# Kernel tuning notes

Measured on AMD Instinct MI355X. Metric: run time of the kernel, lower is better.

Reference implementation:

```python
import jax, jax.numpy as jnp
import numpy as np

N = 50000      # nodes
C = 64         # in_channels
O = 64         # out_channels (== in_channels, required by zeros_like in original)
S = 8          # size: number of weight matrices
E = 1700000    # edges (neighbor pairs incl. self-loops), avg degree ~34


def setup_inputs() -> dict:
    key = jax.random.key(0)
    ks = jax.random.split(key, 9)
    node_tensor = jax.random.normal(ks[0], (N, C), dtype=jnp.float32)
    src = jax.random.randint(ks[1], (E,), 0, N)                 # neighbor node j
    dst = jnp.sort(jax.random.randint(ks[2], (E,), 0, N))       # center node i
    sc = 1.0 / np.sqrt(C)
    W = jax.random.normal(ks[3], (S, C, O), dtype=jnp.float32) * sc   # linears weights
    b = jax.random.normal(ks[4], (S, O), dtype=jnp.float32) * sc      # linears biases
    Ws = jax.random.normal(ks[5], (C, S), dtype=jnp.float32) * sc     # source proj
    bs = jax.random.normal(ks[6], (S,), dtype=jnp.float32) * sc
    Wt = jax.random.normal(ks[7], (C, S), dtype=jnp.float32) * sc     # target proj
    bt = jax.random.normal(ks[8], (S,), dtype=jnp.float32) * sc
    return dict(node_tensor=node_tensor, src=src, dst=dst,
                W=W, b=b, Ws=Ws, bs=bs, Wt=Wt, bt=bt)


def reference(node_tensor, src, dst, W, b, Ws, bs, Wt, bt):
    # Per-node soft-assignment logits (FeaStNet)
    s = node_tensor @ Ws + bs          # [N, S] : source_tensor
    t = node_tensor @ Wt + bt          # [N, S] : target_tensor
    # Per-edge assignment: softmax over the `size` dim of source[center] + target[neighbor]
    q = jax.nn.softmax(s[dst] + t[src], axis=-1)      # [E, S]
    # Per-matrix projected node features: weighted[m] = x @ W_m + b_m
    Wx = jnp.einsum('nc,sco->sno', node_tensor, W) + b[:, None, :]   # [S, N, O]
    # msg[e] = sum_m q[e,m] * Wx[m, src[e]]; loop over small fixed S to avoid [S,E,O] blowup
    msg = q[:, 0:1] * Wx[0][src]                      # [E, O]
    for m in range(1, S):
        msg = msg + q[:, m:m + 1] * Wx[m][src]
    # Scatter-sum over each center's neighborhood, mean over the S weight matrices
    out = jax.ops.segment_sum(msg, dst, num_segments=N) / S          # [N, O]
    return out
```

## Files before the change

kernel.cpp:

```cpp
#include <hip/hip_runtime.h>
#include <hip/hip_bf16.h>


#define CDIM 64
#define SDIM 8

typedef __bf16 bf16x8 __attribute__((ext_vector_type(8)));
typedef __bf16 bf16x4 __attribute__((ext_vector_type(4)));
typedef float f32x4 __attribute__((ext_vector_type(4)));

__global__ __launch_bounds__(256) void k1_pre(
    const float* __restrict__ x, const float* __restrict__ Ws,
    const float* __restrict__ bs, const float* __restrict__ Wt,
    const float* __restrict__ bt, const float* __restrict__ W,
    const int* __restrict__ dst, float* __restrict__ ST,
    __hip_bfloat16* __restrict__ xbf, __hip_bfloat16* __restrict__ WtB,
    int* __restrict__ rowptr, int N, int E, int nbN) {
  int bid = blockIdx.x;
  if (bid >= nbN + 128) {
    int e = (bid - nbN - 128) * 256 + threadIdx.x;
    if (e >= E) return;
    int a = dst[e];
    int bnd = (e + 1 < E) ? dst[e + 1] : N;
    if (e == 0) {
      for (int d = 0; d <= a; ++d) rowptr[d] = 0;
    }
    for (int d = a + 1; d <= bnd; ++d) rowptr[d] = e + 1;
    return;
  }
  if (bid >= nbN) {
    int t = (bid - nbN) * 256 + threadIdx.x;
    int o = t >> 9, k = t & 511;
    WtB[t] = __float2bfloat16(W[(size_t)k * 64 + o]);
    return;
  }

  __shared__ __hip_bfloat16 wst[16 * 72];
  __shared__ float bst[16];
  int t = threadIdx.x;
#pragma unroll
  for (int j = 0; j < 4; ++j) {
    int idx = t * 4 + j;
    int n = idx >> 6, k = idx & 63;
    float v = (n < 8) ? Ws[k * 8 + n] : Wt[k * 8 + (n - 8)];
    wst[n * 72 + k] = __float2bfloat16(v);
  }
  if (t < 16) bst[t] = (t < 8) ? bs[t] : bt[t - 8];
  __syncthreads();

  int wave = t >> 6, lane = t & 63;
  int r = lane & 15, q = lane >> 4;
  int node = bid * 64 + wave * 16 + r;
  int nodec = node < N ? node : N - 1;
  const float* xr = x + (size_t)nodec * CDIM;

  bf16x8 afrag[2];
#pragma unroll
  for (int kt = 0; kt < 2; ++kt) {
    float4 u0 = *(const float4*)(xr + kt * 32 + q * 8);
    float4 u1 = *(const float4*)(xr + kt * 32 + q * 8 + 4);
    union { bf16x8 v; __hip_bfloat16 h[8]; } a;
    a.h[0] = __float2bfloat16(u0.x); a.h[1] = __float2bfloat16(u0.y);
    a.h[2] = __float2bfloat16(u0.z); a.h[3] = __float2bfloat16(u0.w);
    a.h[4] = __float2bfloat16(u1.x); a.h[5] = __float2bfloat16(u1.y);
    a.h[6] = __float2bfloat16(u1.z); a.h[7] = __float2bfloat16(u1.w);
    afrag[kt] = a.v;
    if (node < N)
      *(bf16x8*)(xbf + (size_t)node * CDIM + kt * 32 + q * 8) = a.v;
  }

  bf16x8 bf0 = *(const bf16x8*)(wst + r * 72 + q * 8);
  bf16x8 bf1 = *(const bf16x8*)(wst + r * 72 + 32 + q * 8);

  f32x4 acc = {0, 0, 0, 0};
  acc = __builtin_amdgcn_mfma_f32_16x16x32_bf16(afrag[0], bf0, acc, 0, 0, 0);
  acc = __builtin_amdgcn_mfma_f32_16x16x32_bf16(afrag[1], bf1, acc, 0, 0, 0);

  int m = lane & 15;
#pragma unroll
  for (int v = 0; v < 4; ++v) {
    int nd = bid * 64 + wave * 16 + q * 4 + v;
    if (nd >= N) continue;
    float val = acc[v] + bst[m];
    if (m >= 8) val = __expf(val);
    ST[nd * 16 + m] = val;
  }
}

__global__ __launch_bounds__(256, 4) void k3_mfma(
    const __hip_bfloat16* __restrict__ xbf, const int* __restrict__ src,
    const int* __restrict__ rowptr, const float* __restrict__ ST,
    __hip_bfloat16* __restrict__ Gbf, float* __restrict__ R, int N) {
  __shared__ __hip_bfloat16 qt_s[4][16 * 40];
  __shared__ __hip_bfloat16 xt_s[4][4 * 32 * 16];

  int wave = threadIdx.x >> 6;
  int lane = threadIdx.x & 63;
  int i = blockIdx.x * 4 + wave;
  if (i >= N) return;

  int mm = lane & 7;
  int kk = lane >> 3;
  int mp = lane & 15;
  int q3 = lane >> 4;

  __hip_bfloat16* qt = &qt_s[wave][0];
  __hip_bfloat16* xt = &xt_s[wave][0];

  __hip_bfloat16 z0 = __float2bfloat16(0.0f);
#pragma unroll
  for (int z = 0; z < 5; ++z) qt[320 + z * 64 + lane] = z0;

  int lo = rowptr[i];
  int hi = rowptr[i + 1];
  float uv = __expf(ST[i * 16 + mm]);

  unsigned rd_addr = (unsigned)(uintptr_t)xt + (unsigned)q3 * 256u +
                     (unsigned)mp * 8u;
  __hip_bfloat16* xw = xt + (mm >> 1) * 512 + (mm & 1) * 8;

  f32x4 acc0 = {0, 0, 0, 0}, acc1 = {0, 0, 0, 0};
  f32x4 acc2 = {0, 0, 0, 0}, acc3 = {0, 0, 0, 0};
  float racc = 0.f;

  if (lo < hi) {
    int ecl = hi - 1;
    int iv[4], niv[4];
    bf16x8 xv[4];
    float tv[4];

#pragma unroll
    for (int g = 0; g < 4; ++g) {
      int ek = lo + g * 8 + kk;
      iv[g] = src[ek < ecl ? ek : ecl];
    }
#pragma unroll
    for (int g = 0; g < 4; ++g)
      xv[g] = *(const bf16x8*)(xbf + (size_t)iv[g] * CDIM + mm * 8);
#pragma unroll
    for (int g = 0; g < 4; ++g) tv[g] = ST[iv[g] * 16 + 8 + mm];
    if (lo + 32 < hi) {
#pragma unroll
      for (int g = 0; g < 4; ++g) {
        int ek = lo + 32 + g * 8 + kk;
        niv[g] = src[ek < ecl ? ek : ecl];
      }
    }

    for (int c0 = lo; c0 < hi; c0 += 32) {
      bool hasn = (c0 + 32 < hi);
      bf16x8 nxv[4];
      float ntv[4];
      int nniv[4];
      if (hasn) {
#pragma unroll
        for (int g = 0; g < 4; ++g)
          nxv[g] = *(const bf16x8*)(xbf + (size_t)niv[g] * CDIM + mm * 8);
#pragma unroll
        for (int g = 0; g < 4; ++g) ntv[g] = ST[niv[g] * 16 + 8 + mm];
        if (c0 + 64 < hi) {
#pragma unroll
          for (int g = 0; g < 4; ++g) {
            int ek = c0 + 64 + g * 8 + kk;
            nniv[g] = src[ek < ecl ? ek : ecl];
          }
        }
      }

#pragma unroll
      for (int g = 0; g < 4; ++g) {
        float w = uv * tv[g];
        float ssum = w + __shfl_xor(w, 1);
        ssum += __shfl_xor(ssum, 2);
        ssum += __shfl_xor(ssum, 4);
        float qv = w * __frcp_rn(ssum);
        if (c0 + g * 8 + kk >= hi) qv = 0.f;
        racc += qv;
        qt[mm * 40 + g * 8 + kk] = __float2bfloat16(qv);
      }

#pragma unroll
      for (int g = 0; g < 4; ++g)
        *(bf16x8*)(xw + (g * 8 + kk) * 16) = xv[g];

      bf16x8 afrag = *(const bf16x8*)(qt + mp * 40 + q3 * 8);

      bf16x4 t0, t1, t2, t3, t4, t5, t6, t7;
      asm volatile(
          "ds_read_b64_tr_b16 %0, %8 offset:0\n\t"
          "ds_read_b64_tr_b16 %1, %8 offset:128\n\t"
          "ds_read_b64_tr_b16 %2, %8 offset:1024\n\t"
          "ds_read_b64_tr_b16 %3, %8 offset:1152\n\t"
          "ds_read_b64_tr_b16 %4, %8 offset:2048\n\t"
          "ds_read_b64_tr_b16 %5, %8 offset:2176\n\t"
          "ds_read_b64_tr_b16 %6, %8 offset:3072\n\t"
          "ds_read_b64_tr_b16 %7, %8 offset:3200"
          : "=&v"(t0), "=&v"(t1), "=&v"(t2), "=&v"(t3),
            "=&v"(t4), "=&v"(t5), "=&v"(t6), "=&v"(t7)
          : "v"(rd_addr)
          : "memory");
      asm volatile("s_waitcnt lgkmcnt(0)" ::: "memory");
      __builtin_amdgcn_sched_barrier(0);

      union { bf16x8 v; bf16x4 h[2]; } b0, b1, b2, b3;
      b0.h[0] = t0; b0.h[1] = t1;
      b1.h[0] = t2; b1.h[1] = t3;
      b2.h[0] = t4; b2.h[1] = t5;
      b3.h[0] = t6; b3.h[1] = t7;

      acc0 = __builtin_amdgcn_mfma_f32_16x16x32_bf16(afrag, b0.v, acc0, 0, 0, 0);
      acc1 = __builtin_amdgcn_mfma_f32_16x16x32_bf16(afrag, b1.v, acc1, 0, 0, 0);
      acc2 = __builtin_amdgcn_mfma_f32_16x16x32_bf16(afrag, b2.v, acc2, 0, 0, 0);
      acc3 = __builtin_amdgcn_mfma_f32_16x16x32_bf16(afrag, b3.v, acc3, 0, 0, 0);

      if (hasn) {
#pragma unroll
        for (int g = 0; g < 4; ++g) {
          iv[g] = niv[g];
          xv[g] = nxv[g];
          tv[g] = ntv[g];
          niv[g] = nniv[g];
        }
      }
    }
  }

  if (q3 < 2) {
    __hip_bfloat16* Gi = Gbf + (size_t)i * 512;
#pragma unroll
    for (int v = 0; v < 4; ++v) {
      int m = q3 * 4 + v;
      Gi[m * 64 + 0 + mp]  = __float2bfloat16(acc0[v]);
      Gi[m * 64 + 16 + mp] = __float2bfloat16(acc1[v]);
      Gi[m * 64 + 32 + mp] = __float2bfloat16(acc2[v]);
      Gi[m * 64 + 48 + mp] = __float2bfloat16(acc3[v]);
    }
  }

  racc += __shfl_xor(racc, 8);
  racc += __shfl_xor(racc, 16);
  racc += __shfl_xor(racc, 32);
  if (lane < 8) R[(size_t)i * 8 + lane] = racc;
}

__global__ __launch_bounds__(1024) void k4_mfma(
    const __hip_bfloat16* __restrict__ Gbf, const float* __restrict__ R,
    const __hip_bfloat16* __restrict__ WtB, const float* __restrict__ bias,
    float* __restrict__ out, int N) {
  __shared__ float4 btile[64 * 65];
  {
    const float4* srcp = (const float4*)WtB;
    int t = threadIdx.x;
#pragma unroll
    for (int j = 0; j < 4; ++j) {
      int ci = t + j * 1024;
      btile[(ci >> 6) * 65 + (ci & 63)] = srcp[ci];
    }
  }
  __syncthreads();

  int wave = threadIdx.x >> 6;
  int lane = threadIdx.x & 63;
  int r0 = (blockIdx.x * 16 + wave) * 16;
  if (r0 >= N) return;

  int m = lane & 15;
  int q = lane >> 4;
  const __bf16* abase = (const __bf16*)(Gbf + (size_t)(r0 + m) * 512) + q * 8;
  const __bf16* lbase = (const __bf16*)btile + (size_t)m * 520 + q * 8;

  f32x4 acc0 = {0, 0, 0, 0}, acc1 = {0, 0, 0, 0};
  f32x4 acc2 = {0, 0, 0, 0}, acc3 = {0, 0, 0, 0};
#pragma unroll
  for (int kt = 0; kt < 16; ++kt) {
    bf16x8 a = *(const bf16x8*)(abase + kt * 32);
    bf16x8 b0 = *(const bf16x8*)(lbase + 0 * 520 + kt * 32);
    bf16x8 b1 = *(const bf16x8*)(lbase + 16 * 520 + kt * 32);
    bf16x8 b2 = *(const bf16x8*)(lbase + 32 * 520 + kt * 32);
    bf16x8 b3 = *(const bf16x8*)(lbase + 48 * 520 + kt * 32);
    acc0 = __builtin_amdgcn_mfma_f32_16x16x32_bf16(a, b0, acc0, 0, 0, 0);
    acc1 = __builtin_amdgcn_mfma_f32_16x16x32_bf16(a, b1, acc1, 0, 0, 0);
    acc2 = __builtin_amdgcn_mfma_f32_16x16x32_bf16(a, b2, acc2, 0, 0, 0);
    acc3 = __builtin_amdgcn_mfma_f32_16x16x32_bf16(a, b3, acc3, 0, 0, 0);
  }

#pragma unroll
  for (int v = 0; v < 4; ++v) {
    int ri = r0 + q * 4 + v;
    if (ri >= N) continue;
    const float* Ri = R + (size_t)ri * 8;
    float b0s = 0, b1s = 0, b2s = 0, b3s = 0;
#pragma unroll
    for (int mm = 0; mm < 8; ++mm) {
      float rv = Ri[mm];
      b0s = fmaf(rv, bias[mm * 64 + 0 + m], b0s);
      b1s = fmaf(rv, bias[mm * 64 + 16 + m], b1s);
      b2s = fmaf(rv, bias[mm * 64 + 32 + m], b2s);
      b3s = fmaf(rv, bias[mm * 64 + 48 + m], b3s);
    }
    float* orow = out + (size_t)ri * 64;
    orow[0 + m]  = (acc0[v] + b0s) * 0.125f;
    orow[16 + m] = (acc1[v] + b1s) * 0.125f;
    orow[32 + m] = (acc2[v] + b2s) * 0.125f;
    orow[48 + m] = (acc3[v] + b3s) * 0.125f;
  }
}

extern "C" void kernel_launch(void* const* d_in, const int* in_sizes, int n_in,
                              void* d_out, int out_size, void* d_ws, size_t ws_size,
                              hipStream_t stream) {
  const float* x  = (const float*)d_in[0];
  const int* src  = (const int*)d_in[1];
  const int* dst  = (const int*)d_in[2];
  const float* W  = (const float*)d_in[3];
  const float* b  = (const float*)d_in[4];
  const float* Ws = (const float*)d_in[5];
  const float* bs = (const float*)d_in[6];
  const float* Wt = (const float*)d_in[7];
  const float* bt = (const float*)d_in[8];
  int N = in_sizes[0] / CDIM;
  int E = in_sizes[1];
  float* out = (float*)d_out;

  float* ST = (float*)d_ws;
  __hip_bfloat16* Gbf = (__hip_bfloat16*)(ST + (size_t)N * 16);
  float* R  = (float*)(Gbf + (size_t)N * 512);
  __hip_bfloat16* WtB = (__hip_bfloat16*)(R + (size_t)N * 8);
  __hip_bfloat16* xbf = WtB + 64 * 512;
  int* rowptr = (int*)(xbf + (size_t)N * CDIM);

  int nbN = (N + 63) / 64;
  int nbE = (E + 255) / 256;
  k1_pre<<<nbN + 128 + nbE, 256, 0, stream>>>(x, Ws, bs, Wt, bt, W, dst, ST,
                                              xbf, WtB, rowptr, N, E, nbN);
  k3_mfma<<<(N + 3) / 4, 256, 0, stream>>>(xbf, src, rowptr, ST, Gbf, R, N);
  int mtiles = (N + 15) / 16;
  k4_mfma<<<(mtiles + 15) / 16, 1024, 0, stream>>>(Gbf, R, WtB, b, out, N);
}
```

Before: 158.6 us.

## Store exp target logits in compact bf16 and tile G for coalesced MFMA loads

k1 now also writes a compact bf16 copy of the exponentiated target logits (8 per node), which k3 gathers instead of the strided fp32 ST entries, cutting the bytes per random gather. The G intermediate is relaid out in 16-row tiles arranged in MFMA fragment order, so each lane in k4 reads contiguous 16-byte chunks at kt*512 stride rather than row-strided data. In exchange, k3's stores become more scattered, and the bf16 rounding of exp(t) adds some precision error to the softmax weights.

Result: no change. 159.4 us (+0.5%).

```diff
diff --git a/kernel.cpp b/kernel.cpp
--- a/kernel.cpp
+++ b/kernel.cpp
@@ -14,8 +14,9 @@
     const float* __restrict__ bs, const float* __restrict__ Wt,
     const float* __restrict__ bt, const float* __restrict__ W,
     const int* __restrict__ dst, float* __restrict__ ST,
-    __hip_bfloat16* __restrict__ xbf, __hip_bfloat16* __restrict__ WtB,
-    int* __restrict__ rowptr, int N, int E, int nbN) {
+    __hip_bfloat16* __restrict__ ETb, __hip_bfloat16* __restrict__ xbf,
+    __hip_bfloat16* __restrict__ WtB, int* __restrict__ rowptr,
+    int N, int E, int nbN) {
   int bid = blockIdx.x;
   if (bid >= nbN + 128) {
     int e = (bid - nbN - 128) * 256 + threadIdx.x;
@@ -82,7 +83,10 @@
     int nd = bid * 64 + wave * 16 + q * 4 + v;
     if (nd >= N) continue;
     float val = acc[v] + bst[m];
-    if (m >= 8) val = __expf(val);
+    if (m >= 8) {
+      val = __expf(val);
+      ETb[(size_t)nd * 8 + (m - 8)] = __float2bfloat16(val);
+    }
     ST[nd * 16 + m] = val;
   }
 }
@@ -90,6 +94,7 @@
 __global__ __launch_bounds__(256, 4) void k3_mfma(
     const __hip_bfloat16* __restrict__ xbf, const int* __restrict__ src,
     const int* __restrict__ rowptr, const float* __restrict__ ST,
+    const __hip_bfloat16* __restrict__ ETb,
     __hip_bfloat16* __restrict__ Gbf, float* __restrict__ R, int N) {
   __shared__ __hip_bfloat16 qt_s[4][16 * 40];
   __shared__ __hip_bfloat16 xt_s[4][4 * 32 * 16];
@@ -138,7 +143,8 @@
     for (int g = 0; g < 4; ++g)
       xv[g] = *(const bf16x8*)(xbf + (size_t)iv[g] * CDIM + mm * 8);
 #pragma unroll
-    for (int g = 0; g < 4; ++g) tv[g] = ST[iv[g] * 16 + 8 + mm];
+    for (int g = 0; g < 4; ++g)
+      tv[g] = __bfloat162float(ETb[(size_t)iv[g] * 8 + mm]);
     if (lo + 32 < hi) {
 #pragma unroll
       for (int g = 0; g < 4; ++g) {
@@ -157,7 +163,8 @@
         for (int g = 0; g < 4; ++g)
           nxv[g] = *(const bf16x8*)(xbf + (size_t)niv[g] * CDIM + mm * 8);
 #pragma unroll
-        for (int g = 0; g < 4; ++g) ntv[g] = ST[niv[g] * 16 + 8 + mm];
+        for (int g = 0; g < 4; ++g)
+          ntv[g] = __bfloat162float(ETb[(size_t)niv[g] * 8 + mm]);
         if (c0 + 64 < hi) {
 #pragma unroll
           for (int g = 0; g < 4; ++g) {
@@ -226,14 +233,16 @@
   }
 
   if (q3 < 2) {
-    __hip_bfloat16* Gi = Gbf + (size_t)i * 512;
+    __hip_bfloat16* GT = Gbf + (size_t)(i >> 4) * 8192 + (i & 15) * 8 + (mp & 7);
+    int qh = (mp >> 3) * 128;
 #pragma unroll
     for (int v = 0; v < 4; ++v) {
       int m = q3 * 4 + v;
-      Gi[m * 64 + 0 + mp]  = __float2bfloat16(acc0[v]);
-      Gi[m * 64 + 16 + mp] = __float2bfloat16(acc1[v]);
-      Gi[m * 64 + 32 + mp] = __float2bfloat16(acc2[v]);
-      Gi[m * 64 + 48 + mp] = __float2bfloat16(acc3[v]);
+      __hip_bfloat16* g0 = GT + (2 * m) * 512 + qh;
+      g0[0]         = __float2bfloat16(acc0[v]);
+      g0[256]       = __float2bfloat16(acc1[v]);
+      g0[512]       = __float2bfloat16(acc2[v]);
+      g0[512 + 256] = __float2bfloat16(acc3[v]);
     }
   }
 
@@ -261,19 +270,20 @@
 
   int wave = threadIdx.x >> 6;
   int lane = threadIdx.x & 63;
-  int r0 = (blockIdx.x * 16 + wave) * 16;
+  int Tw = blockIdx.x * 16 + wave;
+  int r0 = Tw * 16;
   if (r0 >= N) return;
 
   int m = lane & 15;
   int q = lane >> 4;
-  const __bf16* abase = (const __bf16*)(Gbf + (size_t)(r0 + m) * 512) + q * 8;
+  const __bf16* abase = (const __bf16*)Gbf + (size_t)Tw * 8192 + lane * 8;
   const __bf16* lbase = (const __bf16*)btile + (size_t)m * 520 + q * 8;
 
   f32x4 acc0 = {0, 0, 0, 0}, acc1 = {0, 0, 0, 0};
   f32x4 acc2 = {0, 0, 0, 0}, acc3 = {0, 0, 0, 0};
 #pragma unroll
   for (int kt = 0; kt < 16; ++kt) {
-    bf16x8 a = *(const bf16x8*)(abase + kt * 32);
+    bf16x8 a = *(const bf16x8*)(abase + kt * 512);
     bf16x8 b0 = *(const bf16x8*)(lbase + 0 * 520 + kt * 32);
     bf16x8 b1 = *(const bf16x8*)(lbase + 16 * 520 + kt * 32);
     bf16x8 b2 = *(const bf16x8*)(lbase + 32 * 520 + kt * 32);
@@ -322,18 +332,20 @@
   int E = in_sizes[1];
   float* out = (float*)d_out;
 
+  int NT = (N + 15) / 16;
   float* ST = (float*)d_ws;
   __hip_bfloat16* Gbf = (__hip_bfloat16*)(ST + (size_t)N * 16);
-  float* R  = (float*)(Gbf + (size_t)N * 512);
+  float* R  = (float*)(Gbf + (size_t)NT * 8192);
   __hip_bfloat16* WtB = (__hip_bfloat16*)(R + (size_t)N * 8);
   __hip_bfloat16* xbf = WtB + 64 * 512;
-  int* rowptr = (int*)(xbf + (size_t)N * CDIM);
+  __hip_bfloat16* ETb = xbf + (size_t)N * CDIM;
+  int* rowptr = (int*)(ETb + (size_t)N * 8);
 
   int nbN = (N + 63) / 64;
   int nbE = (E + 255) / 256;
   k1_pre<<<nbN + 128 + nbE, 256, 0, stream>>>(x, Ws, bs, Wt, bt, W, dst, ST,
-                                              xbf, WtB, rowptr, N, E, nbN);
-  k3_mfma<<<(N + 3) / 4, 256, 0, stream>>>(xbf, src, rowptr, ST, Gbf, R, N);
-  int mtiles = (N + 15) / 16;
+                                              ETb, xbf, WtB, rowptr, N, E, nbN);
+  k3_mfma<<<(N + 3) / 4, 256, 0, stream>>>(xbf, src, rowptr, ST, ETb, Gbf, R, N);
+  int mtiles = NT;
   k4_mfma<<<(mtiles + 15) / 16, 1024, 0, stream>>>(Gbf, R, WtB, b, out, N);
 }
```
